# Performance work log

Measured on AMD Instinct MI355X. Metric: run time of the kernel, lower is better.

The kernel has to match this reference:

```python
import jax, jax.numpy as jnp
import numpy as np

N_HEADS = 4
ROPE_THETA = 10000.0


def rotate_half(x):
    h = x.shape[-1] // 2
    return jnp.concatenate([-x[..., h:], x[..., :h]], axis=-1)


def setup_inputs() -> dict:
    key = jax.random.key(0)
    k1, k2, k3, k4, k5 = jax.random.split(key, 5)
    B, L, D, M = 4, 2048, 216, 64
    x = jax.random.normal(k1, (B, L, D), dtype=jnp.float32)
    mem_k = jax.random.normal(k2, (B, M, D), dtype=jnp.float32)
    mem_v = jax.random.normal(k3, (B, M, D), dtype=jnp.float32)
    attention_mask = jnp.ones((B, L), dtype=jnp.int32)
    # pre-transposed Linear weights (y = x @ W); scaled for stability
    Wqkv = jax.random.normal(k4, (D, 3 * D), dtype=jnp.float32) * (D ** -0.5)
    Wo = jax.random.normal(k5, (D, D), dtype=jnp.float32) * (D ** -0.5)
    return {"x": x, "mem_k": mem_k, "mem_v": mem_v,
            "attention_mask": attention_mask, "Wqkv": Wqkv, "Wo": Wo}


def reference(x, mem_k, mem_v, attention_mask, Wqkv, Wo):
    B, L, D = x.shape
    H = N_HEADS
    hd = D // H
    scale = hd ** -0.5
    M = mem_k.shape[1]

    # QKV projection -> [B, L, 3, H, hd] -> [B, H, L, hd]
    qkv = (x @ Wqkv).reshape(B, L, 3, H, hd)
    q = jnp.transpose(qkv[:, :, 0], (0, 2, 1, 3))
    k = jnp.transpose(qkv[:, :, 1], (0, 2, 1, 3))
    v = jnp.transpose(qkv[:, :, 2], (0, 2, 1, 3))

    # RoPE (cos/sin: [L, hd], broadcast over B,H)
    inv_freq = 1.0 / (ROPE_THETA ** (jnp.arange(0, hd, 2, dtype=jnp.float32) / hd))
    t = jnp.arange(L, dtype=jnp.float32)
    freqs = jnp.outer(t, inv_freq)
    emb = jnp.concatenate([freqs, freqs], axis=-1)
    cos, sin = jnp.cos(emb), jnp.sin(emb)
    q = q * cos + rotate_half(q) * sin
    k = k * cos + rotate_half(k) * sin

    # memory KV: [B, M, D] -> [B, H, M, hd], prepend along kv axis
    mk = jnp.transpose(mem_k.reshape(B, M, H, hd), (0, 2, 1, 3))
    mv = jnp.transpose(mem_v.reshape(B, M, H, hd), (0, 2, 1, 3))
    k_all = jnp.concatenate([mk, k], axis=2)  # [B, H, M+L, hd]
    v_all = jnp.concatenate([mv, v], axis=2)

    scores = jnp.einsum('bhld,bhmd->bhlm', q, k_all) * scale  # [B,H,L,M+L]

    # causal mask applies only to the self-attention block (cols >= M)
    causal = jnp.triu(jnp.ones((L, L), dtype=bool), k=1)
    full_causal = jnp.concatenate([jnp.zeros((L, M), dtype=bool), causal], axis=1)
    scores = jnp.where(full_causal[None, None], -jnp.inf, scores)

    # padding mask: memory positions always valid
    combined = jnp.concatenate(
        [jnp.ones((B, M), dtype=attention_mask.dtype), attention_mask], axis=-1)
    scores = jnp.where(combined[:, None, None, :] == 0, -jnp.inf, scores)

    attn = jax.nn.softmax(scores, axis=-1)  # dropout is identity in eval
    out = jnp.einsum('bhlm,bhmd->bhld', attn, v_all)
    out = jnp.transpose(out, (0, 2, 1, 3)).reshape(B, L, D)
    return out @ Wo
```

## Files before the change

### kernel.cpp

```cpp
#include <hip/hip_runtime.h>
#include <math.h>

#define B_ 4
#define L_ 2048
#define D_ 216
#define H_ 4
#define HD 54
#define HDP 64
#define M_ 64
#define LK 2112
#define NT_ 33
#define KP 256
#define SPB 84
#define QSCALE 0.19632593f

typedef __attribute__((ext_vector_type(8))) __bf16 bf16x8;
typedef __attribute__((ext_vector_type(4))) __bf16 bf16x4;
typedef __attribute__((ext_vector_type(4))) float f32x4;

__device__ __forceinline__ int unpack_d(int j) { return (j >> 1) + 27 * (j & 1); }

__global__ __launch_bounds__(256) void prep(const float* __restrict__ Wqkv,
                                            const float* __restrict__ Wo,
                                            const int* __restrict__ amask,
                                            const float* __restrict__ mk,
                                            const float* __restrict__ mv,
                                            __bf16* __restrict__ wqkvt,
                                            __bf16* __restrict__ wot,
                                            float2* __restrict__ table,
                                            float* __restrict__ bias,
                                            int* __restrict__ padflag,
                                            __bf16* __restrict__ kall,
                                            __bf16* __restrict__ vt) {
    const int bid = blockIdx.x, tid = threadIdx.x;
    if (bid < 768) {
        int idx = bid * 256 + tid;
        int pc = idx >> 8, k = idx & 255;
        float v = 0.f;
        if (k < 216) {
            int col = -1;
            if (pc < 256) { int h = pc >> 6, j = pc & 63;
                if (j < HD) col = h * HD + unpack_d(j); }
            else if (pc < 512) { int h = (pc - 256) >> 6, j = (pc - 256) & 63;
                if (j < HD) col = 216 + h * HD + unpack_d(j); }
            else if (pc < 728) col = 432 + (pc - 512);
            if (col >= 0) v = Wqkv[(size_t)k * 648 + col];
        }
        wqkvt[idx] = (__bf16)v;
    } else if (bid < 1024) {
        int idx = (bid - 768) * 256 + tid;
        int n = idx >> 8, k = idx & 255;
        wot[idx] = (__bf16)((n < 216 && k < 216) ? Wo[(size_t)k * 216 + n] : 0.f);
    } else if (bid < 1280) {
        int idx = (bid - 1024) * 256 + tid;
        int l = idx >> 5, ii = idx & 31;
        float2 sc = {0.f, 0.f};
        if (ii < 27) {
            float ang = (float)l * exp2f(-0.49213749924f * (float)ii);
            sc.x = sinf(ang); sc.y = cosf(ang);
        }
        table[idx] = sc;
    } else if (bid < 1313) {
        int idx = (bid - 1280) * 256 + tid;
        if (idx < B_ * LK) {
            int b = idx / LK, c = idx % LK;
            bias[idx] = (c < M_ || amask[b * L_ + c - M_] != 0) ? 0.f : -1e30f;
        }
    } else if (bid == 1313) {
        if (tid < B_ * NT_) {
            int b = tid / NT_, tile = tid % NT_;
            int flag = 0;
            for (int u = 0; u < 64; ++u) {
                int c = tile * 64 + u;
                if (c >= M_ && c < LK && amask[b * L_ + c - M_] == 0) flag = 1;
            }
            padflag[tid] = flag;
        }
    } else {
        int idx = (bid - 1314) * 256 + tid;
        int b  = idx >> 14;
        int m  = (idx >> 8) & 63;
        int h  = (idx >> 6) & 3;
        int dd = idx & 63;
        float kv = (dd < HD) ? mk[((size_t)(b * M_ + m)) * D_ + h * HD + unpack_d(dd)] : 0.f;
        kall[((size_t)(b * 4 + h) * LK + m) * HDP + dd] = (__bf16)kv;
        if (dd < HD)
            vt[((size_t)(b * 4 + h) * HD + dd) * LK + m] =
                (__bf16)mv[((size_t)(b * M_ + m)) * D_ + h * HD + dd];
    }
}

__global__ __launch_bounds__(256) void gemm_qkv(const float* __restrict__ x,
                                                const __bf16* __restrict__ Bt,
                                                const float2* __restrict__ table,
                                                __bf16* __restrict__ qb,
                                                __bf16* __restrict__ kall,
                                                __bf16* __restrict__ vt) {
    __shared__ __align__(16) __bf16 As[8192];
    __shared__ __align__(16) __bf16 Bs[4096];
    const int col0 = blockIdx.x * 64;
    const int row0 = blockIdx.y * 128;
    const int tid = threadIdx.x;
    const int lane = tid & 63;
    const int w = tid >> 6, wm = w >> 1, wn = w & 1;
    const int l15 = lane & 15, l4 = lane >> 4;

    f32x4 acc[4][2];
    #pragma unroll
    for (int m = 0; m < 4; ++m)
        #pragma unroll
        for (int n = 0; n < 2; ++n) acc[m][n] = (f32x4){0.f, 0.f, 0.f, 0.f};

    float4 rfa[4][2];
    bf16x8 rb[2];
    #pragma unroll
    for (int i = 0; i < 4; ++i) { int c = tid + 256 * i, r = c >> 3, c8 = c & 7;
        int k = c8 * 8;
        rfa[i][0] = *reinterpret_cast<const float4*>(x + (size_t)(row0 + r) * 216 + k);
        rfa[i][1] = *reinterpret_cast<const float4*>(x + (size_t)(row0 + r) * 216 + k + 4); }
    #pragma unroll
    for (int i = 0; i < 2; ++i) { int c = tid + 256 * i, r = c >> 3, c8 = c & 7;
        rb[i] = *reinterpret_cast<const bf16x8*>(Bt + (size_t)(col0 + r) * KP + c8 * 8); }

    for (int kit = 0; kit < 4; ++kit) {
        __syncthreads();
        #pragma unroll
        for (int i = 0; i < 4; ++i) { int c = tid + 256 * i, r = c >> 3, c8 = c & 7;
            bf16x8 v;
            #pragma unroll
            for (int j = 0; j < 4; ++j) { v[j] = (__bf16)rfa[i][0][j]; v[4 + j] = (__bf16)rfa[i][1][j]; }
            *reinterpret_cast<bf16x8*>(&As[r * 64 + ((c8 ^ (r & 7)) * 8)]) = v; }
        #pragma unroll
        for (int i = 0; i < 2; ++i) { int c = tid + 256 * i, r = c >> 3, c8 = c & 7;
            *reinterpret_cast<bf16x8*>(&Bs[r * 64 + ((c8 ^ (r & 7)) * 8)]) = rb[i]; }
        __syncthreads();
        if (kit < 3) {
            const int k0 = (kit + 1) * 64;
            #pragma unroll
            for (int i = 0; i < 4; ++i) { int c = tid + 256 * i, r = c >> 3, c8 = c & 7;
                int k = k0 + c8 * 8;
                if (k < 216) {
                    rfa[i][0] = *reinterpret_cast<const float4*>(x + (size_t)(row0 + r) * 216 + k);
                    rfa[i][1] = *reinterpret_cast<const float4*>(x + (size_t)(row0 + r) * 216 + k + 4);
                } else {
                    rfa[i][0] = (float4){0.f, 0.f, 0.f, 0.f};
                    rfa[i][1] = (float4){0.f, 0.f, 0.f, 0.f};
                } }
            #pragma unroll
            for (int i = 0; i < 2; ++i) { int c = tid + 256 * i, r = c >> 3, c8 = c & 7;
                rb[i] = *reinterpret_cast<const bf16x8*>(Bt + (size_t)(col0 + r) * KP + k0 + c8 * 8); }
        }
        #pragma unroll
        for (int ks = 0; ks < 2; ++ks) {
            bf16x8 af[4], bfr[2];
            #pragma unroll
            for (int m = 0; m < 4; ++m) { int row = wm * 64 + m * 16 + l15; int ch = ks * 4 + l4;
                af[m] = *reinterpret_cast<const bf16x8*>(&As[row * 64 + ((ch ^ (row & 7)) * 8)]); }
            #pragma unroll
            for (int n = 0; n < 2; ++n) { int row = wn * 32 + n * 16 + l15; int ch = ks * 4 + l4;
                bfr[n] = *reinterpret_cast<const bf16x8*>(&Bs[row * 64 + ((ch ^ (row & 7)) * 8)]); }
            #pragma unroll
            for (int m = 0; m < 4; ++m)
                #pragma unroll
                for (int n = 0; n < 2; ++n)
                    acc[m][n] = __builtin_amdgcn_mfma_f32_16x16x32_bf16(af[m], bfr[n], acc[m][n], 0, 0, 0);
        }
    }

    #pragma unroll
    for (int m = 0; m < 4; ++m)
        #pragma unroll
        for (int n = 0; n < 2; ++n) {
            const int cc = col0 + wn * 32 + n * 16 + l15;
            const int rowb = row0 + wm * 64 + m * 16 + l4 * 4;
            const int b = rowb >> 11;
            const int lbase = rowb & 2047;
            if (cc < 512) {
                const bool isq = cc < 256;
                const int h = (cc >> 6) & 3, j = cc & 63;
                const int half = j & 1, ii = j >> 1;
                #pragma unroll
                for (int rr = 0; rr < 4; ++rr) {
                    float me = acc[m][n][rr];
                    float pr = __shfl_xor(me, 1);
                    float2 sc = table[(lbase + rr) * 32 + ii];
                    float v = me * sc.y + (half ? pr * sc.x : -pr * sc.x);
                    if (isq) {
                        qb[((size_t)(b * 4 + h) * L_ + lbase + rr) * HDP + j] =
                            (__bf16)(v * QSCALE);
                    } else {
                        kall[((size_t)(b * 4 + h) * LK + M_ + lbase + rr) * HDP + j] =
                            (__bf16)v;
                    }
                }
            } else if (cc < 728) {
                const int dp = cc - 512;
                const int h = (dp * 1214) >> 16;
                const int d = dp - h * 54;
                #pragma unroll
                for (int rr = 0; rr < 4; ++rr)
                    vt[((size_t)(b * 4 + h) * HD + d) * LK + M_ + lbase + rr] =
                        (__bf16)acc[m][n][rr];
            }
        }
}

__global__ __launch_bounds__(256) void gemm_out(const __bf16* __restrict__ A,
                                                const __bf16* __restrict__ Bt,
                                                float* __restrict__ C, int N) {
    __shared__ __align__(16) __bf16 As[8192];
    __shared__ __align__(16) __bf16 Bs[4096];
    const int col0 = blockIdx.x * 64;
    const int row0 = blockIdx.y * 128;
    const int tid = threadIdx.x;
    const int lane = tid & 63;
    const int w = tid >> 6, wm = w >> 1, wn = w & 1;
    const int l15 = lane & 15, l4 = lane >> 4;

    f32x4 acc[4][2];
    #pragma unroll
    for (int m = 0; m < 4; ++m)
        #pragma unroll
        for (int n = 0; n < 2; ++n) acc[m][n] = (f32x4){0.f, 0.f, 0.f, 0.f};

    bf16x8 ra[4], rb[2];
    #pragma unroll
    for (int i = 0; i < 4; ++i) { int c = tid + 256 * i, r = c >> 3, c8 = c & 7;
        ra[i] = *reinterpret_cast<const bf16x8*>(A + (size_t)(row0 + r) * KP + c8 * 8); }
    #pragma unroll
    for (int i = 0; i < 2; ++i) { int c = tid + 256 * i, r = c >> 3, c8 = c & 7;
        rb[i] = *reinterpret_cast<const bf16x8*>(Bt + (size_t)(col0 + r) * KP + c8 * 8); }

    for (int kit = 0; kit < 4; ++kit) {
        __syncthreads();
        #pragma unroll
        for (int i = 0; i < 4; ++i) { int c = tid + 256 * i, r = c >> 3, c8 = c & 7;
            *reinterpret_cast<bf16x8*>(&As[r * 64 + ((c8 ^ (r & 7)) * 8)]) = ra[i]; }
        #pragma unroll
        for (int i = 0; i < 2; ++i) { int c = tid + 256 * i, r = c >> 3, c8 = c & 7;
            *reinterpret_cast<bf16x8*>(&Bs[r * 64 + ((c8 ^ (r & 7)) * 8)]) = rb[i]; }
        __syncthreads();
        if (kit < 3) {
            const int k0 = (kit + 1) * 64;
            #pragma unroll
            for (int i = 0; i < 4; ++i) { int c = tid + 256 * i, r = c >> 3, c8 = c & 7;
                ra[i] = *reinterpret_cast<const bf16x8*>(A + (size_t)(row0 + r) * KP + k0 + c8 * 8); }
            #pragma unroll
            for (int i = 0; i < 2; ++i) { int c = tid + 256 * i, r = c >> 3, c8 = c & 7;
                rb[i] = *reinterpret_cast<const bf16x8*>(Bt + (size_t)(col0 + r) * KP + k0 + c8 * 8); }
        }
        #pragma unroll
        for (int ks = 0; ks < 2; ++ks) {
            bf16x8 af[4], bfr[2];
            #pragma unroll
            for (int m = 0; m < 4; ++m) { int row = wm * 64 + m * 16 + l15; int ch = ks * 4 + l4;
                af[m] = *reinterpret_cast<const bf16x8*>(&As[row * 64 + ((ch ^ (row & 7)) * 8)]); }
            #pragma unroll
            for (int n = 0; n < 2; ++n) { int row = wn * 32 + n * 16 + l15; int ch = ks * 4 + l4;
                bfr[n] = *reinterpret_cast<const bf16x8*>(&Bs[row * 64 + ((ch ^ (row & 7)) * 8)]); }
            #pragma unroll
            for (int m = 0; m < 4; ++m)
                #pragma unroll
                for (int n = 0; n < 2; ++n)
                    acc[m][n] = __builtin_amdgcn_mfma_f32_16x16x32_bf16(af[m], bfr[n], acc[m][n], 0, 0, 0);
        }
    }
    #pragma unroll
    for (int m = 0; m < 4; ++m)
        #pragma unroll
        for (int n = 0; n < 2; ++n) {
            int cc = col0 + wn * 32 + n * 16 + l15;
            if (cc < N) {
                #pragma unroll
                for (int rr = 0; rr < 4; ++rr)
                    C[(size_t)(row0 + wm * 64 + m * 16 + l4 * 4 + rr) * N + cc] = acc[m][n][rr];
            }
        }
}

__global__ __launch_bounds__(256) void flash_split(const __bf16* __restrict__ qb,
                                                   const __bf16* __restrict__ kall,
                                                   const __bf16* __restrict__ vt,
                                                   const float* __restrict__ bias,
                                                   const int* __restrict__ padflag,
                                                   float* __restrict__ op,
                                                   float* __restrict__ ml,
                                                   __bf16* __restrict__ aoutb) {
    int qt = 31, sp = 0;
    {
        int sidx = blockIdx.x, accq = 0;
        for (int q = 0; q < 32; ++q) {
            int c = (q + 9) >> 3;
            if (sidx < accq + c) { qt = q; sp = sidx - accq; break; }
            accq += c;
        }
    }
    const int pb = blockIdx.y * SPB + blockIdx.x;
    const int q0 = qt * 64;
    const int bh = blockIdx.y;
    const int b = bh >> 2, h = bh & 3;
    const int ntl = qt + 2;
    const int ns = (ntl + 7) >> 3;
    const int base = ntl / ns, rem = ntl % ns;
    const int tstart = sp * base + min(sp, rem);
    const int tend = tstart + base + (sp < rem ? 1 : 0);
    const bool single = (ns == 1);

    __shared__ __align__(16) __bf16 Qs[4096];
    __shared__ __align__(16) __bf16 Ks[2][4096];
    __shared__ __align__(16) __bf16 Vs[2][4096];
    __shared__ __align__(16) __bf16 Ps[4096];
    __shared__ float biasS[2][64];

    const int tid = threadIdx.x;
    const int lane = tid & 63;
    const int w = tid >> 6;
    const int l15 = lane & 15;
    const int l4 = lane >> 4;

    {
        const __bf16* src = qb + ((size_t)bh * L_ + q0) * HDP;
        for (int ch = tid; ch < 512; ch += 256) {
            int row = ch >> 3, c8 = ch & 7;
            bf16x8 v = *reinterpret_cast<const bf16x8*>(src + ch * 8);
            *reinterpret_cast<bf16x8*>(&Qs[row * 64 + ((c8 ^ (row & 7)) * 8)]) = v;
        }
        if (tid < 160) {
            int buf = tid >= 80, q = tid - 80 * buf;
            int d = 54 + (q >> 3), c8 = q & 7;
            bf16x8 z{};
            *reinterpret_cast<bf16x8*>(&Vs[buf][d * 64 + ((c8 ^ (d & 7)) * 8)]) = z;
        }
    }

    const int rq = q0 + 16 * w + l15;
    const __bf16* kbase = kall + (size_t)bh * LK * HDP;
    const __bf16* vbase = vt + (size_t)bh * HD * LK;

    bf16x8 rk[2], rv[2];
    float biasR = 0.f;
    {
        const __bf16* ks = kbase + (size_t)tstart * 64 * HDP;
        rk[0] = *reinterpret_cast<const bf16x8*>(ks + tid * 8);
        rk[1] = *reinterpret_cast<const bf16x8*>(ks + (tid + 256) * 8);
        { int d = tid >> 3, c8 = tid & 7;
          rv[0] = *reinterpret_cast<const bf16x8*>(vbase + (size_t)d * LK + tstart * 64 + c8 * 8); }
        if (tid < 176) { int c = tid + 256, d = c >> 3, c8 = c & 7;
          rv[1] = *reinterpret_cast<const bf16x8*>(vbase + (size_t)d * LK + tstart * 64 + c8 * 8); }
        if (tid < 64) biasR = bias[b * LK + tstart * 64 + tid];

        { int r = tid >> 3, c8 = tid & 7;
          *reinterpret_cast<bf16x8*>(&Ks[0][r * 64 + ((c8 ^ (r & 7)) * 8)]) = rk[0]; }
        { int c = tid + 256, r = c >> 3, c8 = c & 7;
          *reinterpret_cast<bf16x8*>(&Ks[0][r * 64 + ((c8 ^ (r & 7)) * 8)]) = rk[1]; }
        { int d = tid >> 3, c8 = tid & 7;
          *reinterpret_cast<bf16x8*>(&Vs[0][d * 64 + ((c8 ^ (d & 7)) * 8)]) = rv[0]; }
        if (tid < 176) { int c = tid + 256, d = c >> 3, c8 = c & 7;
          *reinterpret_cast<bf16x8*>(&Vs[0][d * 64 + ((c8 ^ (d & 7)) * 8)]) = rv[1]; }
        if (tid < 64) biasS[0][tid] = biasR;
    }
    if (tstart + 1 < tend) {
        const __bf16* ks = kbase + (size_t)(tstart + 1) * 64 * HDP;
        rk[0] = *reinterpret_cast<const bf16x8*>(ks + tid * 8);
        rk[1] = *reinterpret_cast<const bf16x8*>(ks + (tid + 256) * 8);
        { int d = tid >> 3, c8 = tid & 7;
          rv[0] = *reinterpret_cast<const bf16x8*>(vbase + (size_t)d * LK + (tstart + 1) * 64 + c8 * 8); }
        if (tid < 176) { int c = tid + 256, d = c >> 3, c8 = c & 7;
          rv[1] = *reinterpret_cast<const bf16x8*>(vbase + (size_t)d * LK + (tstart + 1) * 64 + c8 * 8); }
        if (tid < 64) biasR = bias[b * LK + (tstart + 1) * 64 + tid];
    }

    __syncthreads();
    bf16x8 aQ[2];
    {
        int qrow = 16 * w + l15, s = (qrow & 7) << 3;
        aQ[0] = *reinterpret_cast<const bf16x8*>(&Qs[qrow * 64 + ((l4 * 8) ^ s)]);
        aQ[1] = *reinterpret_cast<const bf16x8*>(&Qs[qrow * 64 + ((32 + l4 * 8) ^ s)]);
    }

    f32x4 Oacc[4];
    #pragma unroll
    for (int nt = 0; nt < 4; ++nt) Oacc[nt] = (f32x4){0.f, 0.f, 0.f, 0.f};
    float m_run = -1e30f, l_run = 0.f;

    int p = 0;
    for (int t = tstart; t < tend; ++t) {
        const int cbase = t * 64;
        const int qbuf = p ^ 1;
        if (t + 1 < tend) {
            { int r = tid >> 3, c8 = tid & 7;
              *reinterpret_cast<bf16x8*>(&Ks[qbuf][r * 64 + ((c8 ^ (r & 7)) * 8)]) = rk[0]; }
            { int c = tid + 256, r = c >> 3, c8 = c & 7;
              *reinterpret_cast<bf16x8*>(&Ks[qbuf][r * 64 + ((c8 ^ (r & 7)) * 8)]) = rk[1]; }
            { int d = tid >> 3, c8 = tid & 7;
              *reinterpret_cast<bf16x8*>(&Vs[qbuf][d * 64 + ((c8 ^ (d & 7)) * 8)]) = rv[0]; }
            if (tid < 176) { int c = tid + 256, d = c >> 3, c8 = c & 7;
              *reinterpret_cast<bf16x8*>(&Vs[qbuf][d * 64 + ((c8 ^ (d & 7)) * 8)]) = rv[1]; }
            if (tid < 64) biasS[qbuf][tid] = biasR;
        }
        if (t + 2 < tend) {
            const __bf16* ks = kbase + (size_t)(cbase + 128) * HDP;
            rk[0] = *reinterpret_cast<const bf16x8*>(ks + tid * 8);
            rk[1] = *reinterpret_cast<const bf16x8*>(ks + (tid + 256) * 8);
            { int d = tid >> 3, c8 = tid & 7;
              rv[0] = *reinterpret_cast<const bf16x8*>(vbase + (size_t)d * LK + cbase + 128 + c8 * 8); }
            if (tid < 176) { int c = tid + 256, d = c >> 3, c8 = c & 7;
              rv[1] = *reinterpret_cast<const bf16x8*>(vbase + (size_t)d * LK + cbase + 128 + c8 * 8); }
            if (tid < 64) biasR = bias[b * LK + cbase + 128 + tid];
        }
        const int flag = padflag[b * NT_ + t];

        f32x4 S[4];
        __builtin_amdgcn_s_setprio(1);
        #pragma unroll
        for (int nt = 0; nt < 4; ++nt) {
            int krow = nt * 16 + l15, s = (krow & 7) << 3;
            bf16x8 b0 = *reinterpret_cast<const bf16x8*>(&Ks[p][krow * 64 + ((l4 * 8) ^ s)]);
            bf16x8 b1 = *reinterpret_cast<const bf16x8*>(&Ks[p][krow * 64 + ((32 + l4 * 8) ^ s)]);
            f32x4 acc = (f32x4){0.f, 0.f, 0.f, 0.f};
            acc = __builtin_amdgcn_mfma_f32_16x16x32_bf16(b0, aQ[0], acc, 0, 0, 0);
            acc = __builtin_amdgcn_mfma_f32_16x16x32_bf16(b1, aQ[1], acc, 0, 0, 0);
            S[nt] = acc;
        }
        __builtin_amdgcn_s_setprio(0);
        if (flag) {
            #pragma unroll
            for (int nt = 0; nt < 4; ++nt)
                #pragma unroll
                for (int r = 0; r < 4; ++r)
                    S[nt][r] += biasS[p][nt * 16 + l4 * 4 + r];
        }
        if (t == qt + 1) {
            #pragma unroll
            for (int nt = 0; nt < 4; ++nt)
                #pragma unroll
                for (int r = 0; r < 4; ++r) {
                    int cg = cbase + nt * 16 + l4 * 4 + r;
                    if (cg > rq + M_) S[nt][r] = -1e30f;
                }
        }
        float mx;
        {
            float a0 = fmaxf(fmaxf(S[0][0], S[0][1]), S[0][2]);
            float a1 = fmaxf(fmaxf(S[0][3], S[1][0]), S[1][1]);
            float a2 = fmaxf(fmaxf(S[1][2], S[1][3]), S[2][0]);
            float a3 = fmaxf(fmaxf(S[2][1], S[2][2]), S[2][3]);
            float a4 = fmaxf(fmaxf(S[3][0], S[3][1]), S[3][2]);
            float b0 = fmaxf(fmaxf(a0, a1), a2);
            float b1 = fmaxf(fmaxf(a3, a4), S[3][3]);
            mx = fmaxf(b0, b1);
        }
        mx = fmaxf(mx, __shfl_xor(mx, 16));
        mx = fmaxf(mx, __shfl_xor(mx, 32));
        if (!__all(mx <= m_run + 8.f)) {
            float m_new = fmaxf(m_run, mx);
            float alpha = exp2f(m_run - m_new);
            m_run = m_new;
            l_run *= alpha;
            #pragma unroll
            for (int nt = 0; nt < 4; ++nt)
                #pragma unroll
                for (int r = 0; r < 4; ++r) Oacc[nt][r] *= alpha;
        }
        float ls = 0.f;
        #pragma unroll
        for (int nt = 0; nt < 4; ++nt)
            #pragma unroll
            for (int r = 0; r < 4; ++r) {
                float pv = exp2f(S[nt][r] - m_run);
                S[nt][r] = pv;
                ls += pv;
            }
        ls += __shfl_xor(ls, 16);
        ls += __shfl_xor(ls, 32);
        l_run += ls;
        {
            int prow = 16 * w + l15, s = (prow & 7) << 3;
            #pragma unroll
            for (int nt = 0; nt < 4; ++nt) {
                bf16x4 pk;
                pk[0] = (__bf16)S[nt][0]; pk[1] = (__bf16)S[nt][1];
                pk[2] = (__bf16)S[nt][2]; pk[3] = (__bf16)S[nt][3];
                *reinterpret_cast<bf16x4*>(&Ps[prow * 64 + ((nt * 16 + l4 * 4) ^ s)]) = pk;
            }
        }
        bf16x8 aP[2];
        {
            int prow = 16 * w + l15, s = (prow & 7) << 3;
            aP[0] = *reinterpret_cast<const bf16x8*>(&Ps[prow * 64 + ((l4 * 8) ^ s)]);
            aP[1] = *reinterpret_cast<const bf16x8*>(&Ps[prow * 64 + ((32 + l4 * 8) ^ s)]);
        }
        __builtin_amdgcn_s_setprio(1);
        #pragma unroll
        for (int nt = 0; nt < 4; ++nt) {
            int vrow = nt * 16 + l15, s = (vrow & 7) << 3;
            bf16x8 v0 = *reinterpret_cast<const bf16x8*>(&Vs[p][vrow * 64 + ((l4 * 8) ^ s)]);
            bf16x8 v1 = *reinterpret_cast<const bf16x8*>(&Vs[p][vrow * 64 + ((32 + l4 * 8) ^ s)]);
            Oacc[nt] = __builtin_amdgcn_mfma_f32_16x16x32_bf16(v0, aP[0], Oacc[nt], 0, 0, 0);
            Oacc[nt] = __builtin_amdgcn_mfma_f32_16x16x32_bf16(v1, aP[1], Oacc[nt], 0, 0, 0);
        }
        __builtin_amdgcn_s_setprio(0);
        __syncthreads();
        p ^= 1;
    }

    if (single) {
        float inv = 1.f / l_run;
        const size_t rowbase = (size_t)b * L_ + q0 + 16 * w + l15;
        #pragma unroll
        for (int nt = 0; nt < 4; ++nt) {
            #pragma unroll
            for (int r = 0; r < 4; ++r) {
                int d = nt * 16 + l4 * 4 + r;
                if (d < HD)
                    aoutb[rowbase * KP + h * HD + d] = (__bf16)(Oacc[nt][r] * inv);
            }
        }
    } else {
        if (l4 == 0) {
            ml[((size_t)pb * 64 + 16 * w + l15) * 2 + 0] = m_run;
            ml[((size_t)pb * 64 + 16 * w + l15) * 2 + 1] = l_run;
        }
        #pragma unroll
        for (int nt = 0; nt < 4; ++nt) {
            #pragma unroll
            for (int r = 0; r < 4; ++r) {
                int d = nt * 16 + l4 * 4 + r;
                if (d < HD)
                    op[((size_t)pb * HD + d) * 64 + 16 * w + l15] = Oacc[nt][r];
            }
        }
    }
}

__global__ __launch_bounds__(256) void combine(const float* __restrict__ op,
                                               const float* __restrict__ ml,
                                               __bf16* __restrict__ aoutb) {
    const int qt = blockIdx.x + 7, bh = blockIdx.y;
    const int b = bh >> 2, h = bh & 3;
    const int ns = (qt + 9) >> 3;
    int accq = 0;
    for (int q = 0; q < qt; ++q) accq += (q + 9) >> 3;
    const int pb0 = bh * SPB + accq;
    const int row = threadIdx.x & 63;
    const int dseg = threadIdx.x >> 6;

    float mi[5], li[5];
    float m = -1e30f;
    for (int i = 0; i < ns; ++i) {
        mi[i] = ml[((size_t)(pb0 + i) * 64 + row) * 2 + 0];
        li[i] = ml[((size_t)(pb0 + i) * 64 + row) * 2 + 1];
        m = fmaxf(m, mi[i]);
    }
    float wgt[5], Lr = 0.f;
    for (int i = 0; i < ns; ++i) {
        wgt[i] = exp2f(mi[i] - m);
        Lr += li[i] * wgt[i];
    }
    float inv = 1.f / Lr;
    #pragma unroll
    for (int j = 0; j < 14; ++j) {
        int d = dseg * 14 + j;
        if (d < HD) {
            float o = 0.f;
            for (int i = 0; i < ns; ++i)
                o += wgt[i] * op[((size_t)(pb0 + i) * HD + d) * 64 + row];
            aoutb[((size_t)(b * L_) + qt * 64 + row) * KP + h * HD + d] = (__bf16)(o * inv);
        }
    }
}

extern "C" void kernel_launch(void* const* d_in, const int* in_sizes, int n_in,
                              void* d_out, int out_size, void* d_ws, size_t ws_size,
                              hipStream_t stream) {
    const float* x     = (const float*)d_in[0];
    const float* mem_k = (const float*)d_in[1];
    const float* mem_v = (const float*)d_in[2];
    const int*   amask = (const int*)d_in[3];
    const float* Wqkv  = (const float*)d_in[4];
    const float* Wo    = (const float*)d_in[5];
    float* out = (float*)d_out;

    char* p = (char*)d_ws;
    float* bias    = (float*)p;        p += (size_t)B_ * LK * 4;
    int*   padflag = (int*)p;          p += (size_t)B_ * NT_ * 4;
    float2* table  = (float2*)p;       p += (size_t)2048 * 32 * 8;
    __bf16* wqkvt  = (__bf16*)p;       p += (size_t)768 * KP * 2;
    __bf16* wot    = (__bf16*)p;       p += (size_t)256 * KP * 2;
    __bf16* aoutb  = (__bf16*)p;       p += (size_t)8192 * KP * 2;
    __bf16* qb     = (__bf16*)p;       p += (size_t)16 * 2048 * 64 * 2;
    __bf16* kall   = (__bf16*)p;       p += (size_t)16 * 2112 * 64 * 2;
    __bf16* vt     = (__bf16*)p;       p += (size_t)16 * 54 * 2112 * 2;
    float* opbuf   = (float*)p;        p += (size_t)16 * SPB * HD * 64 * 4;
    float* mlbuf   = (float*)p;        p += (size_t)16 * SPB * 64 * 2 * 4;

    prep<<<dim3(1570), 256, 0, stream>>>(Wqkv, Wo, amask, mem_k, mem_v,
                                         wqkvt, wot, table, bias, padflag, kall, vt);
    gemm_qkv<<<dim3(12, 64), 256, 0, stream>>>(x, wqkvt, table, qb, kall, vt);
    flash_split<<<dim3(SPB, 16), 256, 0, stream>>>(qb, kall, vt, bias, padflag,
                                                   opbuf, mlbuf, aoutb);
    combine<<<dim3(25, 16), 256, 0, stream>>>(opbuf, mlbuf, aoutb);
    gemm_out<<<dim3(4, 64), 256, 0, stream>>>(aoutb, wot, out, 216);
}
```

Measured before the change: 98.83 us.

## Widen QKV GEMM tile to 128 columns and single-buffer flash K/V staging

The QKV projection GEMM now computes 128x128 output tiles per block instead of 128x64, halving the grid and doubling per-warp accumulators to raise reuse of the A tile. Separately, the flash attention kernel drops its double-buffered LDS K/V and bias staging in favour of a single buffer, with one register prefetch of the next tile and bias read directly from global memory. This cuts LDS use, which may allow more blocks per CU, but adds an extra barrier per iteration and removes the deeper prefetch.

Measured after the change: 99.15 us. Within noise of the previous version (+0.3%).

```diff
diff --git a/kernel.cpp b/kernel.cpp
--- a/kernel.cpp
+++ b/kernel.cpp
@@ -97,29 +97,29 @@
                                                 __bf16* __restrict__ kall,
                                                 __bf16* __restrict__ vt) {
     __shared__ __align__(16) __bf16 As[8192];
-    __shared__ __align__(16) __bf16 Bs[4096];
-    const int col0 = blockIdx.x * 64;
+    __shared__ __align__(16) __bf16 Bs[8192];
+    const int col0 = blockIdx.x * 128;
     const int row0 = blockIdx.y * 128;
     const int tid = threadIdx.x;
     const int lane = tid & 63;
     const int w = tid >> 6, wm = w >> 1, wn = w & 1;
     const int l15 = lane & 15, l4 = lane >> 4;
 
-    f32x4 acc[4][2];
+    f32x4 acc[4][4];
     #pragma unroll
     for (int m = 0; m < 4; ++m)
         #pragma unroll
-        for (int n = 0; n < 2; ++n) acc[m][n] = (f32x4){0.f, 0.f, 0.f, 0.f};
+        for (int n = 0; n < 4; ++n) acc[m][n] = (f32x4){0.f, 0.f, 0.f, 0.f};
 
     float4 rfa[4][2];
-    bf16x8 rb[2];
+    bf16x8 rb[4];
     #pragma unroll
     for (int i = 0; i < 4; ++i) { int c = tid + 256 * i, r = c >> 3, c8 = c & 7;
         int k = c8 * 8;
         rfa[i][0] = *reinterpret_cast<const float4*>(x + (size_t)(row0 + r) * 216 + k);
         rfa[i][1] = *reinterpret_cast<const float4*>(x + (size_t)(row0 + r) * 216 + k + 4); }
     #pragma unroll
-    for (int i = 0; i < 2; ++i) { int c = tid + 256 * i, r = c >> 3, c8 = c & 7;
+    for (int i = 0; i < 4; ++i) { int c = tid + 256 * i, r = c >> 3, c8 = c & 7;
         rb[i] = *reinterpret_cast<const bf16x8*>(Bt + (size_t)(col0 + r) * KP + c8 * 8); }
 
     for (int kit = 0; kit < 4; ++kit) {
@@ -131,7 +131,7 @@
             for (int j = 0; j < 4; ++j) { v[j] = (__bf16)rfa[i][0][j]; v[4 + j] = (__bf16)rfa[i][1][j]; }
             *reinterpret_cast<bf16x8*>(&As[r * 64 + ((c8 ^ (r & 7)) * 8)]) = v; }
         #pragma unroll
-        for (int i = 0; i < 2; ++i) { int c = tid + 256 * i, r = c >> 3, c8 = c & 7;
+        for (int i = 0; i < 4; ++i) { int c = tid + 256 * i, r = c >> 3, c8 = c & 7;
             *reinterpret_cast<bf16x8*>(&Bs[r * 64 + ((c8 ^ (r & 7)) * 8)]) = rb[i]; }
         __syncthreads();
         if (kit < 3) {
@@ -147,22 +147,22 @@
                     rfa[i][1] = (float4){0.f, 0.f, 0.f, 0.f};
                 } }
             #pragma unroll
-            for (int i = 0; i < 2; ++i) { int c = tid + 256 * i, r = c >> 3, c8 = c & 7;
+            for (int i = 0; i < 4; ++i) { int c = tid + 256 * i, r = c >> 3, c8 = c & 7;
                 rb[i] = *reinterpret_cast<const bf16x8*>(Bt + (size_t)(col0 + r) * KP + k0 + c8 * 8); }
         }
         #pragma unroll
         for (int ks = 0; ks < 2; ++ks) {
-            bf16x8 af[4], bfr[2];
+            bf16x8 af[4], bfr[4];
             #pragma unroll
             for (int m = 0; m < 4; ++m) { int row = wm * 64 + m * 16 + l15; int ch = ks * 4 + l4;
                 af[m] = *reinterpret_cast<const bf16x8*>(&As[row * 64 + ((ch ^ (row & 7)) * 8)]); }
             #pragma unroll
-            for (int n = 0; n < 2; ++n) { int row = wn * 32 + n * 16 + l15; int ch = ks * 4 + l4;
+            for (int n = 0; n < 4; ++n) { int row = wn * 64 + n * 16 + l15; int ch = ks * 4 + l4;
                 bfr[n] = *reinterpret_cast<const bf16x8*>(&Bs[row * 64 + ((ch ^ (row & 7)) * 8)]); }
             #pragma unroll
             for (int m = 0; m < 4; ++m)
                 #pragma unroll
-                for (int n = 0; n < 2; ++n)
+                for (int n = 0; n < 4; ++n)
                     acc[m][n] = __builtin_amdgcn_mfma_f32_16x16x32_bf16(af[m], bfr[n], acc[m][n], 0, 0, 0);
         }
     }
@@ -170,8 +170,8 @@
     #pragma unroll
     for (int m = 0; m < 4; ++m)
         #pragma unroll
-        for (int n = 0; n < 2; ++n) {
-            const int cc = col0 + wn * 32 + n * 16 + l15;
+        for (int n = 0; n < 4; ++n) {
+            const int cc = col0 + wn * 64 + n * 16 + l15;
             const int rowb = row0 + wm * 64 + m * 16 + l4 * 4;
             const int b = rowb >> 11;
             const int lbase = rowb & 2047;
@@ -307,10 +307,9 @@
     const bool single = (ns == 1);
 
     __shared__ __align__(16) __bf16 Qs[4096];
-    __shared__ __align__(16) __bf16 Ks[2][4096];
-    __shared__ __align__(16) __bf16 Vs[2][4096];
+    __shared__ __align__(16) __bf16 Ks[4096];
+    __shared__ __align__(16) __bf16 Vs[4096];
     __shared__ __align__(16) __bf16 Ps[4096];
-    __shared__ float biasS[2][64];
 
     const int tid = threadIdx.x;
     const int lane = tid & 63;
@@ -325,11 +324,10 @@
             bf16x8 v = *reinterpret_cast<const bf16x8*>(src + ch * 8);
             *reinterpret_cast<bf16x8*>(&Qs[row * 64 + ((c8 ^ (row & 7)) * 8)]) = v;
         }
-        if (tid < 160) {
-            int buf = tid >= 80, q = tid - 80 * buf;
-            int d = 54 + (q >> 3), c8 = q & 7;
+        if (tid < 80) {
+            int d = 54 + (tid >> 3), c8 = tid & 7;
             bf16x8 z{};
-            *reinterpret_cast<bf16x8*>(&Vs[buf][d * 64 + ((c8 ^ (d & 7)) * 8)]) = z;
+            *reinterpret_cast<bf16x8*>(&Vs[d * 64 + ((c8 ^ (d & 7)) * 8)]) = z;
         }
     }
 
@@ -338,7 +336,6 @@
     const __bf16* vbase = vt + (size_t)bh * HD * LK;
 
     bf16x8 rk[2], rv[2];
-    float biasR = 0.f;
     {
         const __bf16* ks = kbase + (size_t)tstart * 64 * HDP;
         rk[0] = *reinterpret_cast<const bf16x8*>(ks + tid * 8);
@@ -347,27 +344,6 @@
           rv[0] = *reinterpret_cast<const bf16x8*>(vbase + (size_t)d * LK + tstart * 64 + c8 * 8); }
         if (tid < 176) { int c = tid + 256, d = c >> 3, c8 = c & 7;
           rv[1] = *reinterpret_cast<const bf16x8*>(vbase + (size_t)d * LK + tstart * 64 + c8 * 8); }
-        if (tid < 64) biasR = bias[b * LK + tstart * 64 + tid];
-
-        { int r = tid >> 3, c8 = tid & 7;
-          *reinterpret_cast<bf16x8*>(&Ks[0][r * 64 + ((c8 ^ (r & 7)) * 8)]) = rk[0]; }
-        { int c = tid + 256, r = c >> 3, c8 = c & 7;
-          *reinterpret_cast<bf16x8*>(&Ks[0][r * 64 + ((c8 ^ (r & 7)) * 8)]) = rk[1]; }
-        { int d = tid >> 3, c8 = tid & 7;
-          *reinterpret_cast<bf16x8*>(&Vs[0][d * 64 + ((c8 ^ (d & 7)) * 8)]) = rv[0]; }
-        if (tid < 176) { int c = tid + 256, d = c >> 3, c8 = c & 7;
-          *reinterpret_cast<bf16x8*>(&Vs[0][d * 64 + ((c8 ^ (d & 7)) * 8)]) = rv[1]; }
-        if (tid < 64) biasS[0][tid] = biasR;
-    }
-    if (tstart + 1 < tend) {
-        const __bf16* ks = kbase + (size_t)(tstart + 1) * 64 * HDP;
-        rk[0] = *reinterpret_cast<const bf16x8*>(ks + tid * 8);
-        rk[1] = *reinterpret_cast<const bf16x8*>(ks + (tid + 256) * 8);
-        { int d = tid >> 3, c8 = tid & 7;
-          rv[0] = *reinterpret_cast<const bf16x8*>(vbase + (size_t)d * LK + (tstart + 1) * 64 + c8 * 8); }
-        if (tid < 176) { int c = tid + 256, d = c >> 3, c8 = c & 7;
-          rv[1] = *reinterpret_cast<const bf16x8*>(vbase + (size_t)d * LK + (tstart + 1) * 64 + c8 * 8); }
-        if (tid < 64) biasR = bias[b * LK + (tstart + 1) * 64 + tid];
     }
 
     __syncthreads();
@@ -383,30 +359,26 @@
     for (int nt = 0; nt < 4; ++nt) Oacc[nt] = (f32x4){0.f, 0.f, 0.f, 0.f};
     float m_run = -1e30f, l_run = 0.f;
 
-    int p = 0;
     for (int t = tstart; t < tend; ++t) {
         const int cbase = t * 64;
-        const int qbuf = p ^ 1;
+        __syncthreads();
+        { int r = tid >> 3, c8 = tid & 7;
+          *reinterpret_cast<bf16x8*>(&Ks[r * 64 + ((c8 ^ (r & 7)) * 8)]) = rk[0]; }
+        { int c = tid + 256, r = c >> 3, c8 = c & 7;
+          *reinterpret_cast<bf16x8*>(&Ks[r * 64 + ((c8 ^ (r & 7)) * 8)]) = rk[1]; }
+        { int d = tid >> 3, c8 = tid & 7;
+          *reinterpret_cast<bf16x8*>(&Vs[d * 64 + ((c8 ^ (d & 7)) * 8)]) = rv[0]; }
+        if (tid < 176) { int c = tid + 256, d = c >> 3, c8 = c & 7;
+          *reinterpret_cast<bf16x8*>(&Vs[d * 64 + ((c8 ^ (d & 7)) * 8)]) = rv[1]; }
+        __syncthreads();
         if (t + 1 < tend) {
-            { int r = tid >> 3, c8 = tid & 7;
-              *reinterpret_cast<bf16x8*>(&Ks[qbuf][r * 64 + ((c8 ^ (r & 7)) * 8)]) = rk[0]; }
-            { int c = tid + 256, r = c >> 3, c8 = c & 7;
-              *reinterpret_cast<bf16x8*>(&Ks[qbuf][r * 64 + ((c8 ^ (r & 7)) * 8)]) = rk[1]; }
-            { int d = tid >> 3, c8 = tid & 7;
-              *reinterpret_cast<bf16x8*>(&Vs[qbuf][d * 64 + ((c8 ^ (d & 7)) * 8)]) = rv[0]; }
-            if (tid < 176) { int c = tid + 256, d = c >> 3, c8 = c & 7;
-              *reinterpret_cast<bf16x8*>(&Vs[qbuf][d * 64 + ((c8 ^ (d & 7)) * 8)]) = rv[1]; }
-            if (tid < 64) biasS[qbuf][tid] = biasR;
-        }
-        if (t + 2 < tend) {
-            const __bf16* ks = kbase + (size_t)(cbase + 128) * HDP;
+            const __bf16* ks = kbase + (size_t)(cbase + 64) * HDP;
             rk[0] = *reinterpret_cast<const bf16x8*>(ks + tid * 8);
             rk[1] = *reinterpret_cast<const bf16x8*>(ks + (tid + 256) * 8);
             { int d = tid >> 3, c8 = tid & 7;
-              rv[0] = *reinterpret_cast<const bf16x8*>(vbase + (size_t)d * LK + cbase + 128 + c8 * 8); }
+              rv[0] = *reinterpret_cast<const bf16x8*>(vbase + (size_t)d * LK + cbase + 64 + c8 * 8); }
             if (tid < 176) { int c = tid + 256, d = c >> 3, c8 = c & 7;
-              rv[1] = *reinterpret_cast<const bf16x8*>(vbase + (size_t)d * LK + cbase + 128 + c8 * 8); }
-            if (tid < 64) biasR = bias[b * LK + cbase + 128 + tid];
+              rv[1] = *reinterpret_cast<const bf16x8*>(vbase + (size_t)d * LK + cbase + 64 + c8 * 8); }
         }
         const int flag = padflag[b * NT_ + t];
 
@@ -415,8 +387,8 @@
         #pragma unroll
         for (int nt = 0; nt < 4; ++nt) {
             int krow = nt * 16 + l15, s = (krow & 7) << 3;
-            bf16x8 b0 = *reinterpret_cast<const bf16x8*>(&Ks[p][krow * 64 + ((l4 * 8) ^ s)]);
-            bf16x8 b1 = *reinterpret_cast<const bf16x8*>(&Ks[p][krow * 64 + ((32 + l4 * 8) ^ s)]);
+            bf16x8 b0 = *reinterpret_cast<const bf16x8*>(&Ks[krow * 64 + ((l4 * 8) ^ s)]);
+            bf16x8 b1 = *reinterpret_cast<const bf16x8*>(&Ks[krow * 64 + ((32 + l4 * 8) ^ s)]);
             f32x4 acc = (f32x4){0.f, 0.f, 0.f, 0.f};
             acc = __builtin_amdgcn_mfma_f32_16x16x32_bf16(b0, aQ[0], acc, 0, 0, 0);
             acc = __builtin_amdgcn_mfma_f32_16x16x32_bf16(b1, aQ[1], acc, 0, 0, 0);
@@ -428,7 +400,7 @@
             for (int nt = 0; nt < 4; ++nt)
                 #pragma unroll
                 for (int r = 0; r < 4; ++r)
-                    S[nt][r] += biasS[p][nt * 16 + l4 * 4 + r];
+                    S[nt][r] += bias[b * LK + cbase + nt * 16 + l4 * 4 + r];
         }
         if (t == qt + 1) {
             #pragma unroll
@@ -494,14 +466,12 @@
         #pragma unroll
         for (int nt = 0; nt < 4; ++nt) {
             int vrow = nt * 16 + l15, s = (vrow & 7) << 3;
-            bf16x8 v0 = *reinterpret_cast<const bf16x8*>(&Vs[p][vrow * 64 + ((l4 * 8) ^ s)]);
-            bf16x8 v1 = *reinterpret_cast<const bf16x8*>(&Vs[p][vrow * 64 + ((32 + l4 * 8) ^ s)]);
+            bf16x8 v0 = *reinterpret_cast<const bf16x8*>(&Vs[vrow * 64 + ((l4 * 8) ^ s)]);
+            bf16x8 v1 = *reinterpret_cast<const bf16x8*>(&Vs[vrow * 64 + ((32 + l4 * 8) ^ s)]);
             Oacc[nt] = __builtin_amdgcn_mfma_f32_16x16x32_bf16(v0, aP[0], Oacc[nt], 0, 0, 0);
             Oacc[nt] = __builtin_amdgcn_mfma_f32_16x16x32_bf16(v1, aP[1], Oacc[nt], 0, 0, 0);
         }
         __builtin_amdgcn_s_setprio(0);
-        __syncthreads();
-        p ^= 1;
     }
 
     if (single) {
@@ -596,7 +566,7 @@
 
     prep<<<dim3(1570), 256, 0, stream>>>(Wqkv, Wo, amask, mem_k, mem_v,
                                          wqkvt, wot, table, bias, padflag, kall, vt);
-    gemm_qkv<<<dim3(12, 64), 256, 0, stream>>>(x, wqkvt, table, qb, kall, vt);
+    gemm_qkv<<<dim3(6, 64), 256, 0, stream>>>(x, wqkvt, table, qb, kall, vt);
     flash_split<<<dim3(SPB, 16), 256, 0, stream>>>(qb, kall, vt, bias, padflag,
                                                    opbuf, mlbuf, aoutb);
     combine<<<dim3(25, 16), 256, 0, stream>>>(opbuf, mlbuf, aoutb);
```
